# Performance work log

Hardware: AMD Instinct MI355X
Metric: run time of the kernel (lower is better)

## Reference

```python
import jax, jax.numpy as jnp
import numpy as np

B, HI, WI, DIM = 4, 128, 128, 128
HO, WO = HI // 2, WI // 2
NUM_ITERS = 3
EPS_LN, EPS_A = 1e-5, 1e-6


def _nbr_idx(H, W):
    # NATTEN kernel_size=3 neighborhood with border clamping: window center is
    # clip(i, 1, H-2) so every position sees exactly 9 neighbors.
    r = 1
    ci = jnp.clip(jnp.arange(H), r, H - 1 - r)
    cj = jnp.clip(jnp.arange(W), r, W - 1 - r)
    off = jnp.arange(-1, 2)
    ri = ci[:, None] + off[None, :]  # (H,3)
    rj = cj[:, None] + off[None, :]  # (W,3)
    nbr = jnp.broadcast_to(ri[:, None, :, None], (H, W, 3, 3)).reshape(H, W, 9)
    nbc = jnp.broadcast_to(rj[None, :, None, :], (H, W, 3, 3)).reshape(H, W, 9)
    return nbr, nbc


def _ln(x, g, b):
    mu = jnp.mean(x, -1, keepdims=True)
    var = jnp.mean(jnp.square(x - mu), -1, keepdims=True)
    return (x - mu) * jax.lax.rsqrt(var + EPS_LN) * g + b


def setup_inputs() -> dict:
    key = jax.random.key(0)
    ks = jax.random.split(key, 10)
    s = DIM ** -0.5
    return {
        "x": jax.random.normal(ks[0], (B, HI * WI, DIM), jnp.float32),
        "conv_w": jax.random.normal(ks[1], (DIM, DIM, 3, 3), jnp.float32) * (2.0 / (DIM * 9)) ** 0.5,
        "q_w": jax.random.normal(ks[2], (DIM, DIM), jnp.float32) * s,
        "k_w": jax.random.normal(ks[3], (DIM, DIM), jnp.float32) * s,
        "v_w": jax.random.normal(ks[4], (DIM, DIM), jnp.float32) * s,
        "mlp_w1": jax.random.normal(ks[5], (DIM, 2 * DIM), jnp.float32) * s,
        "mlp_b1": jnp.zeros((2 * DIM,), jnp.float32),
        "mlp_w2": jax.random.normal(ks[6], (2 * DIM, DIM), jnp.float32) * (2 * DIM) ** -0.5,
        "mlp_b2": jnp.zeros((DIM,), jnp.float32),
        "ln_in_g": jnp.ones((DIM,), jnp.float32),
        "ln_in_b": jnp.zeros((DIM,), jnp.float32),
        "ln_out_g": jnp.ones((DIM,), jnp.float32),
        "ln_out_b": jnp.zeros((DIM,), jnp.float32),
        "tau": jnp.asarray(np.log(DIM ** -0.5), jnp.float32),
        "rpb": jax.random.normal(ks[7], (4, 9), jnp.float32) * 0.02,
    }


def reference(x, conv_w, q_w, k_w, v_w, mlp_w1, mlp_b1, mlp_w2, mlp_b2,
              ln_in_g, ln_in_b, ln_out_g, ln_out_b, tau, rpb):
    Bx = x.shape[0]
    nbr, nbc = _nbr_idx(HO, WO)
    q_idx = (nbr * WO + nbc).reshape(HO * WO, 9)  # flat seed index of each neighbor

    def to_groups(t):  # (B, Hi*Wi, D) -> (B, 4, Ho, Wo, D); 4 = 2x2 patch pixels (row-major)
        m = t.transpose(0, 2, 1).reshape(Bx, DIM, HO, 2, WO, 2)
        return m.transpose(0, 3, 5, 2, 4, 1).reshape(Bx, 4, HO, WO, DIM)

    k = to_groups(_ln(x, ln_in_g, ln_in_b) @ k_w)
    v = to_groups(x @ v_w)
    v_nb = v[:, :, nbr, nbc, :]  # (B,4,Ho,Wo,9,D) value neighborhoods (loop-invariant)

    x_map = x.transpose(0, 2, 1).reshape(Bx, DIM, HI, WI)
    seed = jax.lax.conv_general_dilated(x_map, conv_w, (2, 2), ((1, 1), (1, 1)),
                                        dimension_numbers=('NCHW', 'OIHW', 'NCHW'))
    x_out = _ln(seed.reshape(Bx, DIM, HO * WO).transpose(0, 2, 1), ln_out_g, ln_out_b)

    scale = jnp.exp(tau)
    flat_idx = jnp.broadcast_to(q_idx[None], (4, HO * WO, 9)).reshape(-1)
    attn = A_col = None
    for _ in range(NUM_ITERS):
        q = _ln(x_out, ln_out_g, ln_out_b) @ q_w
        q_nb = q.reshape(Bx, HO, WO, DIM)[:, nbr, nbc, :]  # (B,Ho,Wo,9,D)
        # na2d_qk(query=k, key=q): logits at key-grid position vs seed neighbors
        attn = jnp.einsum('bghwd,bhwtd->bghwt', k, q_nb)
        attn = jax.nn.softmax((attn + rpb.reshape(1, 4, 1, 1, 9)) * scale, axis=-1) + EPS_A
        # scatter-based column sums over seed tokens (doubly-stochastic step)
        attn_flat = attn.reshape(Bx, -1)
        col_sums = jax.vmap(
            lambda a: jax.ops.segment_sum(a, flat_idx, num_segments=HO * WO))(attn_flat)
        denom = col_sums[:, q_idx]  # (B, Ho*Wo, 9) gather back per-edge
        A_col = (attn.reshape(Bx, 4, HO * WO, 9) / (denom[:, None] + 1e-8)).reshape(Bx, 4, HO, WO, 9)
        # na2d_av(A_col, v) then sum over the 4 patch-pixel groups
        upd = jnp.einsum('bghwt,bghwtd->bhwd', A_col, v_nb).reshape(Bx, HO * WO, DIM)
        x_out = x_out + upd
        h = jax.nn.gelu(x_out @ mlp_w1 + mlp_b1, approximate=False) @ mlp_w2 + mlp_b2
        x_out = x_out + _ln(h, ln_out_g, ln_out_b)
    return x_out, attn, A_col
```

## Files before the change

### kernel.cpp

```cpp
#include <hip/hip_runtime.h>
#include <hip/hip_bf16.h>
#include <math.h>

#define BN 4
#define HIq 128
#define WIq 128
#define DIM 128
#define HOq 64
#define WOq 64
#define NPOS 4096
#define NTOK 16384
#define EPS_LN 1e-5f
#define EPS_A 1e-6f

typedef __attribute__((ext_vector_type(8))) short bf16x8;
typedef __attribute__((ext_vector_type(4))) float f32x4;

__device__ __forceinline__ unsigned short f2bf(float f) {
    unsigned int u = __float_as_uint(f);
    u = (u + 0x7FFFu + ((u >> 16) & 1u)) >> 16;
    return (unsigned short)u;
}

__device__ __forceinline__ float bf2f(unsigned short u) {
    return __uint_as_float((unsigned int)u << 16);
}

__device__ __forceinline__ int nb_index(int h, int w, int t) {
    int ch = min(max(h, 1), HOq - 2);
    int cw = min(max(w, 1), WOq - 2);
    int dr = t / 3 - 1, dc = t % 3 - 1;
    return (ch + dr) * WOq + (cw + dc);
}

__global__ void prep_ln_kernel(const float* __restrict__ x,
                               const float* __restrict__ g,
                               const float* __restrict__ bb,
                               unsigned short* __restrict__ x_bf,
                               unsigned short* __restrict__ xln_bf) {
    int tid = threadIdx.x, wv = tid >> 6, lane = tid & 63;
    long row = (long)blockIdx.x * 4 + wv;
    const float* xr = x + row * DIM;
    float v0 = xr[lane], v1 = xr[lane + 64];
    float s = v0 + v1, ss = v0 * v0 + v1 * v1;
    #pragma unroll
    for (int off = 32; off; off >>= 1) {
        s  += __shfl_xor(s, off, 64);
        ss += __shfl_xor(ss, off, 64);
    }
    float mu = s * (1.0f / DIM);
    float var = fmaxf(ss * (1.0f / DIM) - mu * mu, 0.0f);
    float rstd = rsqrtf(var + EPS_LN);
    x_bf[row * DIM + lane]        = f2bf(v0);
    x_bf[row * DIM + lane + 64]   = f2bf(v1);
    xln_bf[row * DIM + lane]      = f2bf((v0 - mu) * rstd * g[lane] + bb[lane]);
    xln_bf[row * DIM + lane + 64] = f2bf((v1 - mu) * rstd * g[lane + 64] + bb[lane + 64]);
}

__global__ void conv_wt_kernel(const float* __restrict__ cw, unsigned short* __restrict__ wt) {
    int o = blockIdx.x, tap = blockIdx.y, i = threadIdx.x;
    wt[(long)o * 1152 + tap * 128 + i] = f2bf(cw[((long)o * 128 + i) * 9 + tap]);
}

__global__ void wt_all_kernel(const float* __restrict__ kw, const float* __restrict__ vw,
                              const float* __restrict__ qw,
                              const float* __restrict__ w1, const float* __restrict__ w2,
                              unsigned short* __restrict__ kwt, unsigned short* __restrict__ vwt,
                              unsigned short* __restrict__ qwt,
                              unsigned short* __restrict__ w1t, unsigned short* __restrict__ w2t) {
    int o = blockIdx.x, i = threadIdx.x;
    kwt[o * DIM + i] = f2bf(kw[i * DIM + o]);
    vwt[o * DIM + i] = f2bf(vw[i * DIM + o]);
    qwt[o * DIM + i] = f2bf(qw[i * DIM + o]);
    w1t[(2 * o) * DIM + i]     = f2bf(w1[i * 256 + 2 * o]);
    w1t[(2 * o + 1) * DIM + i] = f2bf(w1[i * 256 + 2 * o + 1]);
    w2t[o * 256 + i]       = f2bf(w2[i * DIM + o]);
    w2t[o * 256 + 128 + i] = f2bf(w2[(128 + i) * DIM + o]);
}

__global__ __launch_bounds__(256) void conv_mfma_kernel(
        const unsigned short* __restrict__ x_bf,
        const unsigned short* __restrict__ wt,
        const float* __restrict__ ln_g, const float* __restrict__ ln_b,
        float* __restrict__ out_x) {
    __shared__ __align__(16) char smem[52224];
    unsigned short (*As)[136] = (unsigned short(*)[136])smem;
    unsigned short (*Bs)[136] = (unsigned short(*)[136])(smem + 17408);
    float (*o_s)[132]         = (float(*)[132])smem;

    int tid = threadIdx.x;
    int wv = tid >> 6, lane = tid & 63;
    int quad = lane >> 4, l15 = lane & 15;
    int wr = wv >> 1, wc = wv & 1;
    int b = blockIdx.x >> 6, ho = blockIdx.x & 63;

    f32x4 acc[2][4];
    #pragma unroll
    for (int mt = 0; mt < 2; ++mt)
        #pragma unroll
        for (int nt = 0; nt < 4; ++nt) acc[mt][nt] = (f32x4){0.f, 0.f, 0.f, 0.f};

    for (int tap = 0; tap < 9; ++tap) {
        int kh = tap / 3, kw = tap % 3;
        int hi = 2 * ho - 1 + kh;
        bool hok = (hi >= 0) && (hi < HIq);
        __syncthreads();
        #pragma unroll
        for (int it = 0; it < 4; ++it) {
            int c = it * 256 + tid;
            int row = c >> 4, sg = c & 15;
            int wi = 2 * row - 1 + kw;
            int4 av = {0, 0, 0, 0};
            if (hok && wi >= 0 && wi < WIq)
                av = *(const int4*)(x_bf + (((long)b * HIq + hi) * WIq + wi) * DIM + sg * 8);
            *(int4*)&As[row][sg * 8] = av;
        }
        #pragma unroll
        for (int it = 0; it < 8; ++it) {
            int c = it * 256 + tid;
            int row = c >> 4, sg = c & 15;
            *(int4*)&Bs[row][sg * 8] =
                *(const int4*)(wt + (long)row * 1152 + tap * 128 + sg * 8);
        }
        __syncthreads();
        #pragma unroll
        for (int ib = 0; ib < 4; ++ib) {
            bf16x8 afr[2], bfr[4];
            #pragma unroll
            for (int mt = 0; mt < 2; ++mt)
                afr[mt] = *(bf16x8*)&As[wr * 32 + mt * 16 + l15][ib * 32 + quad * 8];
            #pragma unroll
            for (int nt = 0; nt < 4; ++nt)
                bfr[nt] = *(bf16x8*)&Bs[wc * 64 + nt * 16 + l15][ib * 32 + quad * 8];
            #pragma unroll
            for (int mt = 0; mt < 2; ++mt)
                #pragma unroll
                for (int nt = 0; nt < 4; ++nt)
                    acc[mt][nt] = __builtin_amdgcn_mfma_f32_16x16x32_bf16(
                        afr[mt], bfr[nt], acc[mt][nt], 0, 0, 0);
        }
    }
    __syncthreads();
    #pragma unroll
    for (int mt = 0; mt < 2; ++mt)
        #pragma unroll
        for (int r = 0; r < 4; ++r) {
            int wo = wr * 32 + mt * 16 + quad * 4 + r;
            #pragma unroll
            for (int nt = 0; nt < 4; ++nt) {
                int col = wc * 64 + nt * 16 + l15;
                o_s[wo][col] = acc[mt][nt][r];
            }
        }
    __syncthreads();

    {
        int r = tid >> 2, qq = tid & 3;
        float s = 0.f, ss = 0.f;
        #pragma unroll
        for (int j = 0; j < 32; ++j) {
            float v = o_s[r][qq * 32 + j];
            s += v; ss += v * v;
        }
        s  += __shfl_xor(s, 1, 64);  ss += __shfl_xor(ss, 1, 64);
        s  += __shfl_xor(s, 2, 64);  ss += __shfl_xor(ss, 2, 64);
        float mu = s * (1.0f / DIM);
        float var = fmaxf(ss * (1.0f / DIM) - mu * mu, 0.0f);
        float rstd = rsqrtf(var + EPS_LN);
        long outb = ((long)b * NPOS + ho * WOq) * DIM;
        float* xr = out_x + outb + (long)r * DIM + qq * 32;
        #pragma unroll
        for (int j = 0; j < 32; ++j) {
            int c = qq * 32 + j;
            xr[j] = (o_s[r][c] - mu) * rstd * ln_g[c] + ln_b[c];
        }
    }
}

__global__ __launch_bounds__(256) void kv_mfma_kernel(
        const unsigned short* __restrict__ x_bf,
        const unsigned short* __restrict__ xln_bf,
        const unsigned short* __restrict__ kwt,
        const unsigned short* __restrict__ vwt,
        unsigned short* __restrict__ k_bf, unsigned short* __restrict__ v_bf) {
    __shared__ unsigned short Ak[64][40], Av[64][40];
    __shared__ unsigned short Bk[128][40], Bv[128][40];
    int tid = threadIdx.x;
    int wv = tid >> 6, lane = tid & 63;
    int quad = lane >> 4, l15 = lane & 15;
    int wr = wv >> 1, wc = wv & 1;
    long tokBase = (long)blockIdx.x * 64;

    f32x4 acck[2][4], accv[2][4];
    #pragma unroll
    for (int mt = 0; mt < 2; ++mt)
        #pragma unroll
        for (int nt = 0; nt < 4; ++nt) {
            acck[mt][nt] = (f32x4){0.f, 0.f, 0.f, 0.f};
            accv[mt][nt] = (f32x4){0.f, 0.f, 0.f, 0.f};
        }

    int m = tid >> 2, seg = tid & 3;
    #pragma unroll
    for (int ib = 0; ib < 4; ++ib) {
        __syncthreads();
        *(int4*)&Ak[m][seg * 8] = *(const int4*)(xln_bf + (tokBase + m) * DIM + ib * 32 + seg * 8);
        *(int4*)&Av[m][seg * 8] = *(const int4*)(x_bf   + (tokBase + m) * DIM + ib * 32 + seg * 8);
        #pragma unroll
        for (int r2 = 0; r2 < 2; ++r2) {
            int lin = r2 * 256 + tid;
            int n = lin >> 2, sg = lin & 3;
            *(int4*)&Bk[n][sg * 8] = *(const int4*)(kwt + (long)n * DIM + ib * 32 + sg * 8);
            *(int4*)&Bv[n][sg * 8] = *(const int4*)(vwt + (long)n * DIM + ib * 32 + sg * 8);
        }
        __syncthreads();
        bf16x8 ak[2], av2[2], bk[4], bv[4];
        #pragma unroll
        for (int mt = 0; mt < 2; ++mt) {
            ak[mt]  = *(bf16x8*)&Ak[wr * 32 + mt * 16 + l15][quad * 8];
            av2[mt] = *(bf16x8*)&Av[wr * 32 + mt * 16 + l15][quad * 8];
        }
        #pragma unroll
        for (int nt = 0; nt < 4; ++nt) {
            bk[nt] = *(bf16x8*)&Bk[wc * 64 + nt * 16 + l15][quad * 8];
            bv[nt] = *(bf16x8*)&Bv[wc * 64 + nt * 16 + l15][quad * 8];
        }
        #pragma unroll
        for (int mt = 0; mt < 2; ++mt)
            #pragma unroll
            for (int nt = 0; nt < 4; ++nt) {
                acck[mt][nt] = __builtin_amdgcn_mfma_f32_16x16x32_bf16(ak[mt],  bk[nt], acck[mt][nt], 0, 0, 0);
                accv[mt][nt] = __builtin_amdgcn_mfma_f32_16x16x32_bf16(av2[mt], bv[nt], accv[mt][nt], 0, 0, 0);
            }
    }
    #pragma unroll
    for (int mt = 0; mt < 2; ++mt)
        #pragma unroll
        for (int r = 0; r < 4; ++r) {
            long tok = tokBase + wr * 32 + mt * 16 + quad * 4 + r;
            int b = (int)(tok >> 14);
            int pix = (int)(tok & 16383);
            int ih = pix >> 7, iw = pix & 127;
            int g = (ih & 1) * 2 + (iw & 1);
            int pos = (ih >> 1) * WOq + (iw >> 1);
            long base = ((long)(b * 4 + g) * NPOS + pos) * DIM;
            #pragma unroll
            for (int nt = 0; nt < 4; ++nt) {
                int col = wc * 64 + nt * 16 + l15;
                k_bf[base + col] = f2bf(acck[mt][nt][r]);
                v_bf[base + col] = f2bf(accv[mt][nt][r]);
            }
        }
}

__global__ __launch_bounds__(256) void q_mfma_kernel(
        const float* __restrict__ x_out,
        const unsigned short* __restrict__ qwt,
        const float* __restrict__ ln_g, const float* __restrict__ ln_b,
        unsigned short* __restrict__ q) {
    __shared__ unsigned short sxbf[64][136];
    int tid = threadIdx.x;
    long base = (long)blockIdx.x * 64;

    {
        int r = tid >> 2, qq = tid & 3;
        const float* xr = x_out + (base + r) * DIM + qq * 32;
        float vv[32];
        float s = 0.f, ss = 0.f;
        #pragma unroll
        for (int j = 0; j < 8; ++j) {
            float4 v4 = *(const float4*)(xr + j * 4);
            vv[j * 4 + 0] = v4.x; vv[j * 4 + 1] = v4.y;
            vv[j * 4 + 2] = v4.z; vv[j * 4 + 3] = v4.w;
            s += v4.x + v4.y + v4.z + v4.w;
            ss += v4.x * v4.x + v4.y * v4.y + v4.z * v4.z + v4.w * v4.w;
        }
        s  += __shfl_xor(s, 1, 64);  ss += __shfl_xor(ss, 1, 64);
        s  += __shfl_xor(s, 2, 64);  ss += __shfl_xor(ss, 2, 64);
        float mu = s * (1.0f / DIM);
        float var = fmaxf(ss * (1.0f / DIM) - mu * mu, 0.0f);
        float rstd = rsqrtf(var + EPS_LN);
        #pragma unroll
        for (int j = 0; j < 32; ++j) {
            int c = qq * 32 + j;
            sxbf[r][c] = f2bf((vv[j] - mu) * rstd * ln_g[c] + ln_b[c]);
        }
    }
    __syncthreads();

    int wv = tid >> 6, lane = tid & 63;
    int quad = lane >> 4, l15 = lane & 15;
    f32x4 acc[4][2];
    #pragma unroll
    for (int mt = 0; mt < 4; ++mt)
        #pragma unroll
        for (int nt = 0; nt < 2; ++nt) acc[mt][nt] = (f32x4){0.f, 0.f, 0.f, 0.f};

    #pragma unroll
    for (int kb = 0; kb < 4; ++kb) {
        bf16x8 afr[4], bfr[2];
        #pragma unroll
        for (int mt = 0; mt < 4; ++mt)
            afr[mt] = *(bf16x8*)&sxbf[mt * 16 + l15][kb * 32 + quad * 8];
        #pragma unroll
        for (int nt = 0; nt < 2; ++nt) {
            int n = wv * 32 + nt * 16 + l15;
            bfr[nt] = *(const bf16x8*)(qwt + (long)n * DIM + kb * 32 + quad * 8);
        }
        #pragma unroll
        for (int mt = 0; mt < 4; ++mt)
            #pragma unroll
            for (int nt = 0; nt < 2; ++nt)
                acc[mt][nt] = __builtin_amdgcn_mfma_f32_16x16x32_bf16(
                    afr[mt], bfr[nt], acc[mt][nt], 0, 0, 0);
    }
    #pragma unroll
    for (int mt = 0; mt < 4; ++mt)
        #pragma unroll
        for (int r = 0; r < 4; ++r) {
            long tok = base + mt * 16 + quad * 4 + r;
            #pragma unroll
            for (int nt = 0; nt < 2; ++nt) {
                int col = wv * 32 + nt * 16 + l15;
                q[tok * DIM + col] = f2bf(acc[mt][nt][r]);
            }
        }
}

__global__ void zero_kernel(float* __restrict__ p, int n) {
    int i = blockIdx.x * blockDim.x + threadIdx.x;
    if (i < n) p[i] = 0.0f;
}

__global__ __launch_bounds__(256) void attn_mfma_kernel(
        const unsigned short* __restrict__ k_bf,
        const unsigned short* __restrict__ q_bf,
        const float* __restrict__ rpb,
        const float* __restrict__ tau,
        float* __restrict__ attn_out,
        float* __restrict__ col_sums) {
    __shared__ __align__(16) char smem[69632];
    __shared__ float colacc[192];
    unsigned short (*Ks)[136] = (unsigned short(*)[136])smem;
    unsigned short (*Qs)[136] = (unsigned short(*)[136])(smem + 17408);
    float (*S)[193]           = (float(*)[193])smem;

    int tid = threadIdx.x;
    int bid = blockIdx.x;
    int h = bid & 63, g = (bid >> 6) & 3, b = bid >> 8;
    int r0 = min(max(h, 1), HOq - 2) - 1;

    long kbase = ((long)(b * 4 + g) * NPOS + h * 64) * DIM;
    long qbase = ((long)b * NPOS + r0 * 64) * DIM;

    if (tid < 192) colacc[tid] = 0.f;

    #pragma unroll
    for (int it = 0; it < 4; ++it) {
        int lin = it * 256 + tid;
        int row = lin >> 4, sg = lin & 15;
        *(int4*)&Ks[row][sg * 8] = *(const int4*)(k_bf + kbase + (long)row * DIM + sg * 8);
    }
    #pragma unroll
    for (int it = 0; it < 12; ++it) {
        int lin = it * 256 + tid;
        int row = lin >> 4, sg = lin & 15;
        *(int4*)&Qs[row][sg * 8] = *(const int4*)(q_bf + qbase + (long)row * DIM + sg * 8);
    }
    __syncthreads();

    int wv = tid >> 6, lane = tid & 63;
    int quad = lane >> 4, l15 = lane & 15;
    f32x4 acc[4][3];
    #pragma unroll
    for (int mt = 0; mt < 4; ++mt)
        #pragma unroll
        for (int nt = 0; nt < 3; ++nt) acc[mt][nt] = (f32x4){0.f, 0.f, 0.f, 0.f};

    #pragma unroll
    for (int kb = 0; kb < 4; ++kb) {
        bf16x8 afr[4], bfr[3];
        #pragma unroll
        for (int mt = 0; mt < 4; ++mt)
            afr[mt] = *(bf16x8*)&Ks[mt * 16 + l15][kb * 32 + quad * 8];
        #pragma unroll
        for (int nt = 0; nt < 3; ++nt)
            bfr[nt] = *(bf16x8*)&Qs[wv * 48 + nt * 16 + l15][kb * 32 + quad * 8];
        #pragma unroll
        for (int mt = 0; mt < 4; ++mt)
            #pragma unroll
            for (int nt = 0; nt < 3; ++nt)
                acc[mt][nt] = __builtin_amdgcn_mfma_f32_16x16x32_bf16(
                    afr[mt], bfr[nt], acc[mt][nt], 0, 0, 0);
    }
    __syncthreads();
    #pragma unroll
    for (int mt = 0; mt < 4; ++mt)
        #pragma unroll
        for (int nt = 0; nt < 3; ++nt)
            #pragma unroll
            for (int r = 0; r < 4; ++r)
                S[mt * 16 + quad * 4 + r][wv * 48 + nt * 16 + l15] = acc[mt][nt][r];
    __syncthreads();

    if (tid < 64) {
        int w = tid;
        int cw = min(max(w, 1), WOq - 2);
        float scale = expf(tau[0]);
        float l[9];
        #pragma unroll
        for (int t = 0; t < 9; ++t) {
            int j = (t / 3) * 64 + cw - 1 + (t % 3);
            l[t] = (S[w][j] + rpb[g * 9 + t]) * scale;
        }
        float m = l[0];
        #pragma unroll
        for (int t = 1; t < 9; ++t) m = fmaxf(m, l[t]);
        float e[9], s = 0.f;
        #pragma unroll
        for (int t = 0; t < 9; ++t) { e[t] = __expf(l[t] - m); s += e[t]; }
        float inv = 1.0f / s;
        long cell = (long)(b * 4 + g) * NPOS + h * 64 + w;
        #pragma unroll
        for (int t = 0; t < 9; ++t) {
            float a = e[t] * inv + EPS_A;
            int j = (t / 3) * 64 + cw - 1 + (t % 3);
            attn_out[cell * 9 + t] = a;
            atomicAdd(&colacc[j], a);
        }
    }
    __syncthreads();
    if (tid < 192) atomicAdd(&col_sums[b * NPOS + r0 * 64 + tid], colacc[tid]);
}

__global__ void acol_upd_kernel(const float* __restrict__ attn_out,
                                const float* __restrict__ col_sums,
                                const unsigned short* __restrict__ v_bf,
                                float* __restrict__ acol_out,
                                float* __restrict__ x_out) {
    __shared__ float sA[36];
    int tid = threadIdx.x;
    int row = blockIdx.x;
    int b = row >> 12, pos = row & 4095;
    int h = pos >> 6, w = pos & 63;

    if (tid < 36) {
        int g = tid / 9, t = tid % 9;
        long ci = ((long)(b * 4 + g) * NPOS + pos) * 9 + t;
        float a = attn_out[ci];
        float cs = col_sums[b * NPOS + nb_index(h, w, t)];
        float A = a / (cs + 1e-8f);
        sA[tid] = A;
        acol_out[ci] = A;
    }
    __syncthreads();

    int nn[9];
    #pragma unroll
    for (int t = 0; t < 9; ++t) nn[t] = nb_index(h, w, t);

    float acc = 0.f;
    #pragma unroll
    for (int g = 0; g < 4; ++g) {
        const unsigned short* vb = v_bf + (long)(b * 4 + g) * NPOS * DIM;
        #pragma unroll
        for (int t = 0; t < 9; ++t) {
            acc += sA[g * 9 + t] * bf2f(vb[(long)nn[t] * DIM + tid]);
        }
    }
    x_out[(long)row * DIM + tid] += acc;
}

__global__ __launch_bounds__(256) void mlp_mfma_kernel(
        float* __restrict__ x_out,
        const unsigned short* __restrict__ w1t,
        const unsigned short* __restrict__ w2t,
        const float* __restrict__ b1, const float* __restrict__ b2,
        const float* __restrict__ ln_g, const float* __restrict__ ln_b) {
    __shared__ __align__(16) char smem[51200];
    unsigned short (*sxbf)[136] = (unsigned short(*)[136])smem;
    unsigned short (*h_s)[264]  = (unsigned short(*)[264])(smem + 17408);
    float (*o_s)[132]           = (float(*)[132])smem;

    int tid = threadIdx.x;
    long base = (long)blockIdx.x * 64;
    int wv = tid >> 6, lane = tid & 63;
    int quad = lane >> 4, l15 = lane & 15;

    {
        int r = tid >> 2, seg = tid & 3;
        const float* xr = x_out + (base + r) * DIM + seg * 32;
        #pragma unroll
        for (int j = 0; j < 4; ++j) {
            float4 a = *(const float4*)(xr + j * 8);
            float4 c = *(const float4*)(xr + j * 8 + 4);
            unsigned short u[8] = {f2bf(a.x), f2bf(a.y), f2bf(a.z), f2bf(a.w),
                                   f2bf(c.x), f2bf(c.y), f2bf(c.z), f2bf(c.w)};
            *(int4*)&sxbf[r][seg * 32 + j * 8] = *(int4*)u;
        }
    }
    __syncthreads();

    f32x4 acc1[4][4];
    #pragma unroll
    for (int mt = 0; mt < 4; ++mt)
        #pragma unroll
        for (int nt = 0; nt < 4; ++nt) acc1[mt][nt] = (f32x4){0.f, 0.f, 0.f, 0.f};
    #pragma unroll
    for (int kb = 0; kb < 4; ++kb) {
        bf16x8 afr[4], bfr[4];
        #pragma unroll
        for (int mt = 0; mt < 4; ++mt)
            afr[mt] = *(bf16x8*)&sxbf[mt * 16 + l15][kb * 32 + quad * 8];
        #pragma unroll
        for (int nt = 0; nt < 4; ++nt) {
            int n = wv * 64 + nt * 16 + l15;
            bfr[nt] = *(const bf16x8*)(w1t + (long)n * DIM + kb * 32 + quad * 8);
        }
        #pragma unroll
        for (int mt = 0; mt < 4; ++mt)
            #pragma unroll
            for (int nt = 0; nt < 4; ++nt)
                acc1[mt][nt] = __builtin_amdgcn_mfma_f32_16x16x32_bf16(
                    afr[mt], bfr[nt], acc1[mt][nt], 0, 0, 0);
    }
    #pragma unroll
    for (int nt = 0; nt < 4; ++nt) {
        int col = wv * 64 + nt * 16 + l15;
        float bj = b1[col];
        #pragma unroll
        for (int mt = 0; mt < 4; ++mt)
            #pragma unroll
            for (int r = 0; r < 4; ++r) {
                int row = mt * 16 + quad * 4 + r;
                float hv = acc1[mt][nt][r] + bj;
                hv = 0.5f * hv * (1.0f + erff(hv * 0.70710678118654752f));
                h_s[row][col] = f2bf(hv);
            }
    }
    __syncthreads();

    f32x4 acc2[4][2];
    #pragma unroll
    for (int mt = 0; mt < 4; ++mt)
        #pragma unroll
        for (int nt = 0; nt < 2; ++nt) acc2[mt][nt] = (f32x4){0.f, 0.f, 0.f, 0.f};
    #pragma unroll
    for (int kb = 0; kb < 8; ++kb) {
        bf16x8 afr[4], bfr[2];
        #pragma unroll
        for (int mt = 0; mt < 4; ++mt)
            afr[mt] = *(bf16x8*)&h_s[mt * 16 + l15][kb * 32 + quad * 8];
        #pragma unroll
        for (int nt = 0; nt < 2; ++nt) {
            int n = wv * 32 + nt * 16 + l15;
            bfr[nt] = *(const bf16x8*)(w2t + (long)n * 256 + kb * 32 + quad * 8);
        }
        #pragma unroll
        for (int mt = 0; mt < 4; ++mt)
            #pragma unroll
            for (int nt = 0; nt < 2; ++nt)
                acc2[mt][nt] = __builtin_amdgcn_mfma_f32_16x16x32_bf16(
                    afr[mt], bfr[nt], acc2[mt][nt], 0, 0, 0);
    }
    __syncthreads();

    #pragma unroll
    for (int nt = 0; nt < 2; ++nt) {
        int col = wv * 32 + nt * 16 + l15;
        float bj = b2[col];
        #pragma unroll
        for (int mt = 0; mt < 4; ++mt)
            #pragma unroll
            for (int r = 0; r < 4; ++r)
                o_s[mt * 16 + quad * 4 + r][col] = acc2[mt][nt][r] + bj;
    }
    __syncthreads();

    {
        int r = tid >> 2, qq = tid & 3;
        float s = 0.f, ss = 0.f;
        #pragma unroll
        for (int j = 0; j < 32; ++j) {
            float v = o_s[r][qq * 32 + j];
            s += v; ss += v * v;
        }
        s  += __shfl_xor(s, 1, 64);  ss += __shfl_xor(ss, 1, 64);
        s  += __shfl_xor(s, 2, 64);  ss += __shfl_xor(ss, 2, 64);
        float mu = s * (1.0f / DIM);
        float var = fmaxf(ss * (1.0f / DIM) - mu * mu, 0.0f);
        float rstd = rsqrtf(var + EPS_LN);
        float* xr = x_out + (base + r) * DIM + qq * 32;
        #pragma unroll
        for (int j = 0; j < 32; ++j) {
            int c = qq * 32 + j;
            xr[j] = xr[j] + (o_s[r][c] - mu) * rstd * ln_g[c] + ln_b[c];
        }
    }
}

extern "C" void kernel_launch(void* const* d_in, const int* in_sizes, int n_in,
                              void* d_out, int out_size, void* d_ws, size_t ws_size,
                              hipStream_t stream) {
    const float* x        = (const float*)d_in[0];
    const float* conv_w   = (const float*)d_in[1];
    const float* q_w      = (const float*)d_in[2];
    const float* k_w      = (const float*)d_in[3];
    const float* v_w      = (const float*)d_in[4];
    const float* mlp_w1   = (const float*)d_in[5];
    const float* mlp_b1   = (const float*)d_in[6];
    const float* mlp_w2   = (const float*)d_in[7];
    const float* mlp_b2   = (const float*)d_in[8];
    const float* ln_in_g  = (const float*)d_in[9];
    const float* ln_in_b  = (const float*)d_in[10];
    const float* ln_out_g = (const float*)d_in[11];
    const float* ln_out_b = (const float*)d_in[12];
    const float* tau      = (const float*)d_in[13];
    const float* rpb      = (const float*)d_in[14];

    float* out_x    = (float*)d_out;
    float* out_attn = out_x + (long)BN * NPOS * DIM;
    float* out_acol = out_attn + (long)BN * 4 * NPOS * 9;

    char* ws = (char*)d_ws;
    unsigned short* k_bf = (unsigned short*)ws; ws += (long)BN * 4 * NPOS * DIM * 4;
    unsigned short* v_bf = (unsigned short*)ws; ws += (long)BN * 4 * NPOS * DIM * 4;
    unsigned short* x_bf = (unsigned short*)ws;
    unsigned short* q_bf = (unsigned short*)ws;
    ws += (long)BN * NTOK * DIM * 2;
    unsigned short* xln_bf = (unsigned short*)ws; ws += (long)BN * NTOK * DIM * 2;
    unsigned short* wt_conv = (unsigned short*)ws; ws += 1152L * DIM * 2;
    unsigned short* kwt = (unsigned short*)ws;     ws += (long)DIM * DIM * 2;
    unsigned short* vwt = (unsigned short*)ws;     ws += (long)DIM * DIM * 2;
    unsigned short* qwt = (unsigned short*)ws;     ws += (long)DIM * DIM * 2;
    unsigned short* w1t = (unsigned short*)ws;     ws += 256L * DIM * 2;
    unsigned short* w2t = (unsigned short*)ws;     ws += 256L * DIM * 2;
    float* col_sums = (float*)ws;       ws += (long)BN * NPOS * 4;

    prep_ln_kernel<<<16384, 256, 0, stream>>>(x, ln_in_g, ln_in_b, x_bf, xln_bf);
    conv_wt_kernel<<<dim3(128, 9), 128, 0, stream>>>(conv_w, wt_conv);
    wt_all_kernel<<<128, 128, 0, stream>>>(k_w, v_w, q_w, mlp_w1, mlp_w2,
                                           kwt, vwt, qwt, w1t, w2t);

    kv_mfma_kernel<<<1024, 256, 0, stream>>>(x_bf, xln_bf, kwt, vwt, k_bf, v_bf);
    conv_mfma_kernel<<<256, 256, 0, stream>>>(x_bf, wt_conv, ln_out_g, ln_out_b, out_x);

    for (int it = 0; it < 3; ++it) {
        q_mfma_kernel<<<256, 256, 0, stream>>>(out_x, qwt, ln_out_g, ln_out_b, q_bf);
        zero_kernel<<<(BN * NPOS + 255) / 256, 256, 0, stream>>>(col_sums, BN * NPOS);
        attn_mfma_kernel<<<1024, 256, 0, stream>>>(k_bf, q_bf, rpb, tau, out_attn, col_sums);
        acol_upd_kernel<<<16384, 128, 0, stream>>>(out_attn, col_sums, v_bf, out_acol, out_x);
        mlp_mfma_kernel<<<256, 256, 0, stream>>>(out_x, w1t, w2t, mlp_b1, mlp_b2,
                                                 ln_out_g, ln_out_b);
    }
}
```

Baseline: 324.7 us.

## Tile acol update per output row with shared-memory V staging and XCD-aware block remap

The column-normalise-and-aggregate kernel now processes one full output row (64 positions) per 512-thread block. It stages the three needed V rows per group in shared memory, so each V element is reused across the neighbouring positions instead of being gathered from global memory per position. Block indices in the attention and update kernels are remapped so neighbouring rows land on the same XCD, which should improve L2 reuse. The input LN prep is vectorised to float2 loads and packed bf16 stores. The risk is that only 256 blocks with large LDS use may underfill the GPU.

```diff
diff --git a/kernel.cpp b/kernel.cpp
--- a/kernel.cpp
+++ b/kernel.cpp
@@ -40,9 +40,9 @@
                                unsigned short* __restrict__ xln_bf) {
     int tid = threadIdx.x, wv = tid >> 6, lane = tid & 63;
     long row = (long)blockIdx.x * 4 + wv;
-    const float* xr = x + row * DIM;
-    float v0 = xr[lane], v1 = xr[lane + 64];
-    float s = v0 + v1, ss = v0 * v0 + v1 * v1;
+    const float2* xr = (const float2*)(x + row * DIM);
+    float2 v = xr[lane];
+    float s = v.x + v.y, ss = v.x * v.x + v.y * v.y;
     #pragma unroll
     for (int off = 32; off; off >>= 1) {
         s  += __shfl_xor(s, off, 64);
@@ -51,10 +51,13 @@
     float mu = s * (1.0f / DIM);
     float var = fmaxf(ss * (1.0f / DIM) - mu * mu, 0.0f);
     float rstd = rsqrtf(var + EPS_LN);
-    x_bf[row * DIM + lane]        = f2bf(v0);
-    x_bf[row * DIM + lane + 64]   = f2bf(v1);
-    xln_bf[row * DIM + lane]      = f2bf((v0 - mu) * rstd * g[lane] + bb[lane]);
-    xln_bf[row * DIM + lane + 64] = f2bf((v1 - mu) * rstd * g[lane + 64] + bb[lane + 64]);
+    float2 gg = ((const float2*)g)[lane];
+    float2 bv = ((const float2*)bb)[lane];
+    unsigned int xo = (unsigned int)f2bf(v.x) | ((unsigned int)f2bf(v.y) << 16);
+    *(unsigned int*)&x_bf[row * DIM + 2 * lane] = xo;
+    unsigned int lo = (unsigned int)f2bf((v.x - mu) * rstd * gg.x + bv.x)
+                    | ((unsigned int)f2bf((v.y - mu) * rstd * gg.y + bv.y) << 16);
+    *(unsigned int*)&xln_bf[row * DIM + 2 * lane] = lo;
 }
 
 __global__ void conv_wt_kernel(const float* __restrict__ cw, unsigned short* __restrict__ wt) {
@@ -347,6 +350,7 @@
 
     int tid = threadIdx.x;
     int bid = blockIdx.x;
+    bid = (bid & 7) * 128 + (bid >> 3);
     int h = bid & 63, g = (bid >> 6) & 3, b = bid >> 8;
     int r0 = min(max(h, 1), HOq - 2) - 1;
 
@@ -433,42 +437,65 @@
     if (tid < 192) atomicAdd(&col_sums[b * NPOS + r0 * 64 + tid], colacc[tid]);
 }
 
-__global__ void acol_upd_kernel(const float* __restrict__ attn_out,
-                                const float* __restrict__ col_sums,
-                                const unsigned short* __restrict__ v_bf,
-                                float* __restrict__ acol_out,
-                                float* __restrict__ x_out) {
-    __shared__ float sA[36];
+__global__ __launch_bounds__(512) void acol_upd_kernel(
+        const float* __restrict__ attn_out,
+        const float* __restrict__ col_sums,
+        const unsigned short* __restrict__ v_bf,
+        float* __restrict__ acol_out,
+        float* __restrict__ x_out) {
+    __shared__ unsigned short Vs[3 * 64 * 128];
+    __shared__ float sA[64][9];
+    int bid = blockIdx.x;
+    bid = (bid & 7) * 32 + (bid >> 3);
+    int b = bid >> 6, h = bid & 63;
+    int ch = min(max(h, 1), HOq - 2);
+    int r0 = ch - 1;
     int tid = threadIdx.x;
-    int row = blockIdx.x;
-    int b = row >> 12, pos = row & 4095;
-    int h = pos >> 6, w = pos & 63;
-
-    if (tid < 36) {
-        int g = tid / 9, t = tid % 9;
-        long ci = ((long)(b * 4 + g) * NPOS + pos) * 9 + t;
-        float a = attn_out[ci];
-        float cs = col_sums[b * NPOS + nb_index(h, w, t)];
-        float A = a / (cs + 1e-8f);
-        sA[tid] = A;
-        acol_out[ci] = A;
-    }
-    __syncthreads();
-
-    int nn[9];
-    #pragma unroll
-    for (int t = 0; t < 9; ++t) nn[t] = nb_index(h, w, t);
-
-    float acc = 0.f;
-    #pragma unroll
+    int c = tid & 127, wg4 = tid >> 7;
+
+    float acc[16];
+    #pragma unroll
+    for (int k = 0; k < 16; ++k) acc[k] = 0.f;
+
     for (int g = 0; g < 4; ++g) {
-        const unsigned short* vb = v_bf + (long)(b * 4 + g) * NPOS * DIM;
-        #pragma unroll
-        for (int t = 0; t < 9; ++t) {
-            acc += sA[g * 9 + t] * bf2f(vb[(long)nn[t] * DIM + tid]);
-        }
-    }
-    x_out[(long)row * DIM + tid] += acc;
+        __syncthreads();
+        long vgbase = ((long)(b * 4 + g) * NPOS + r0 * 64) * DIM;
+        #pragma unroll
+        for (int it = 0; it < 6; ++it) {
+            int chunk = it * 512 + tid;
+            int row = chunk >> 4, sg = chunk & 15;
+            *(int4*)&Vs[row * 128 + sg * 8] =
+                *(const int4*)(v_bf + vgbase + (long)row * DIM + sg * 8);
+        }
+        for (int idx = tid; idx < 576; idx += 512) {
+            int w = idx / 9, t = idx % 9;
+            long ci = ((long)(b * 4 + g) * NPOS + h * 64 + w) * 9 + t;
+            float a = attn_out[ci];
+            float cs = col_sums[b * NPOS + nb_index(h, w, t)];
+            float A = a / (cs + 1e-8f);
+            sA[w][t] = A;
+            acol_out[ci] = A;
+        }
+        __syncthreads();
+        #pragma unroll
+        for (int k = 0; k < 16; ++k) {
+            int w = wg4 * 16 + k;
+            int cw = min(max(w, 1), WOq - 2);
+            float a0 = 0.f;
+            #pragma unroll
+            for (int t = 0; t < 9; ++t) {
+                int lrow = (t / 3) * 64 + cw + (t % 3) - 1;
+                a0 += sA[w][t] * bf2f(Vs[lrow * 128 + c]);
+            }
+            acc[k] += a0;
+        }
+    }
+    long xbase = ((long)b * NPOS + h * 64) * DIM;
+    #pragma unroll
+    for (int k = 0; k < 16; ++k) {
+        int w = wg4 * 16 + k;
+        x_out[xbase + (long)w * DIM + c] += acc[k];
+    }
 }
 
 __global__ __launch_bounds__(256) void mlp_mfma_kernel(
@@ -649,7 +676,7 @@
         q_mfma_kernel<<<256, 256, 0, stream>>>(out_x, qwt, ln_out_g, ln_out_b, q_bf);
         zero_kernel<<<(BN * NPOS + 255) / 256, 256, 0, stream>>>(col_sums, BN * NPOS);
         attn_mfma_kernel<<<1024, 256, 0, stream>>>(k_bf, q_bf, rpb, tau, out_attn, col_sums);
-        acol_upd_kernel<<<16384, 128, 0, stream>>>(out_attn, col_sums, v_bf, out_acol, out_x);
+        acol_upd_kernel<<<256, 512, 0, stream>>>(out_attn, col_sums, v_bf, out_acol, out_x);
         mlp_mfma_kernel<<<256, 256, 0, stream>>>(out_x, w1t, w2t, mlp_b1, mlp_b2,
                                                  ln_out_g, ln_out_b);
     }
```

Measured after the change: 345.1 us. 1.06x slower.
